# Kernel tuning notes

Measured on AMD Instinct MI355X. Metric: run time of the kernel, lower is better.

## Reference

```python
import jax, jax.numpy as jnp
import numpy as np
import math

H = 16        # num heads
D = 64        # head dim
HID = 1024    # hidden size
MULT = 2      # GIN MLP multiplier
FRAC = 0.1    # top_k fraction of available predecessors
THR = 0.2     # threshold value
BASE = 10000.0  # rope base
CHUNK = 32    # query-row chunk for max aggregator
NEG = -1e30


def _rope(x, pos):
    # x: (b, H, S, D); pos: (b, S) int
    d = x.shape[-1]
    inv = 1.0 / (BASE ** (jnp.arange(0, d, 2, dtype=jnp.float32) / d))
    ang = pos.astype(jnp.float32)[..., None] * inv            # (b, S, d//2)
    cos = jnp.concatenate([jnp.cos(ang)] * 2, -1)[:, None]    # (b, 1, S, d)
    sin = jnp.concatenate([jnp.sin(ang)] * 2, -1)[:, None]
    x1, x2 = jnp.split(x, 2, axis=-1)
    return x * cos + jnp.concatenate([-x2, x1], -1) * sin


def _scaled_topk_causal(adj):
    # faithful vectorization of scaled_topk_causal_4d: per query row i, keep
    # top max(1, ceil(FRAC*i)) of the (threshold-filtered) strict predecessors.
    S = adj.shape[-1]
    j = jnp.arange(S)
    strict = j[None, :] < j[:, None]                           # (S, S) j < i
    # torch: filtered = a[:, :i] * (a >= thr)  -> below-threshold become 0
    filtered = jnp.where(strict, jnp.where(adj >= THR, adj, 0.0), NEG)
    order = jnp.argsort(-filtered, axis=-1)                    # descending, stable
    rank = jnp.argsort(order, axis=-1)                         # inverse permutation
    k = jnp.maximum(1, jnp.ceil(FRAC * jnp.arange(S, dtype=jnp.float32))).astype(jnp.int32)
    k = k.at[0].set(0)                                         # row 0 has no predecessors
    return ((rank < k[None, None, :, None]) & strict).astype(adj.dtype)


def reference(hidden_states, Wq, Wk, Wv, Wo, W1, W2, eps, position_ids):
    b, S, _ = hidden_states.shape
    q = (hidden_states @ Wq).reshape(b, S, H, D).transpose(0, 2, 1, 3)
    kk = (hidden_states @ Wk).reshape(b, S, H, D).transpose(0, 2, 1, 3)
    v = (hidden_states @ Wv).reshape(b, S, H, D).transpose(0, 2, 1, 3)
    q = _rope(q, position_ids)
    kk = _rope(kk, position_ids)
    scores = jnp.einsum('bhid,bhjd->bhij', q, kk) / math.sqrt(D)
    adj = _scaled_topk_causal(scores)                          # binary (b,H,S,S)
    deg = adj.sum(-1)                                          # (b,H,S)
    denom = jnp.maximum(deg, 1.0)[..., None]
    s_agg = jnp.einsum('bhij,bhjd->bhid', adj, v)              # sum
    m_agg = s_agg / denom                                      # mean
    var = jnp.maximum(jnp.einsum('bhij,bhjd->bhid', adj, v * v) / denom - m_agg ** 2, 0.0)
    # max aggregator: masked max over selected predecessors, chunked over rows
    nc = S // CHUNK
    adj_c = jnp.moveaxis(adj.reshape(b, H, nc, CHUNK, S), 2, 0)  # (nc,b,H,C,S)
    mx = jax.lax.map(
        lambda ac: jnp.max(jnp.where(ac[..., None] > 0, v[:, :, None, :, :], NEG), axis=-2),
        adj_c)                                                 # (nc,b,H,C,D)
    mx = jnp.moveaxis(mx, 0, 2).reshape(b, H, S, D)
    mx = jnp.where(deg[..., None] > 0, mx, 0.0)
    comb = jnp.concatenate([s_agg, m_agg, mx, var], -1)        # (b,H,S,4D)
    h1 = jax.nn.silu(jnp.einsum('bhsf,hfm->bhsm', comb, W1))   # per-head GIN MLP
    head_out = jnp.einsum('bhsm,hmd->bhsd', h1, W2) + eps * v  # epsilon-scaled residual
    return head_out.transpose(0, 2, 1, 3).reshape(b, S, H * D) @ Wo


def setup_inputs() -> dict:
    key = jax.random.key(0)
    ks = jax.random.split(key, 8)
    b, S = 1, 1024
    sc = 0.02
    return {
        'hidden_states': jax.random.normal(ks[0], (b, S, HID), jnp.float32),
        'Wq': jax.random.normal(ks[1], (HID, H * D), jnp.float32) * sc,
        'Wk': jax.random.normal(ks[2], (HID, H * D), jnp.float32) * sc,
        'Wv': jax.random.normal(ks[3], (HID, H * D), jnp.float32) * sc,
        'Wo': jax.random.normal(ks[4], (H * D, HID), jnp.float32) * sc,
        'W1': jax.random.normal(ks[5], (H, 4 * D, MULT * D), jnp.float32) * sc,
        'W2': jax.random.normal(ks[6], (H, MULT * D, D), jnp.float32) * sc,
        'eps': jnp.asarray(0.1, jnp.float32),
        'position_ids': jnp.arange(S, dtype=jnp.int32)[None, :],
    }
```

## Files before the change

kernel.cpp:

```cpp
#include <hip/hip_runtime.h>
#include <math.h>

#define NEGF  -1e30f
#define TAU   1e-6f

static __device__ __forceinline__ int imin(int a, int b) { return a < b ? a : b; }

static __device__ __forceinline__ void fma44(float A[4][4], const float4 xa, const float4 yb) {
  A[0][0] += xa.x * yb.x; A[0][1] += xa.x * yb.y; A[0][2] += xa.x * yb.z; A[0][3] += xa.x * yb.w;
  A[1][0] += xa.y * yb.x; A[1][1] += xa.y * yb.y; A[1][2] += xa.y * yb.z; A[1][3] += xa.y * yb.w;
  A[2][0] += xa.z * yb.x; A[2][1] += xa.z * yb.y; A[2][2] += xa.z * yb.z; A[2][3] += xa.z * yb.w;
  A[3][0] += xa.w * yb.x; A[3][1] += xa.w * yb.y; A[3][2] += xa.w * yb.z; A[3][3] += xa.w * yb.w;
}

static __device__ __forceinline__ void fold44(float T[4][4], float A[4][4]) {
#pragma unroll
  for (int e = 0; e < 4; ++e)
#pragma unroll
    for (int f = 0; f < 4; ++f) { T[e][f] = __fadd_rn(T[e][f], A[e][f]); A[e][f] = 0.0f; }
}

template <int MODE>
__global__ __launch_bounds__(256) void gemm64(
    const float* __restrict__ A, const float* __restrict__ B, float* __restrict__ C,
    const float* __restrict__ R, const float* __restrict__ eps_p,
    int M, int N, int K, int lda, int ldb, int ldc,
    long sA, long sB, long sC)
{
  const int z = blockIdx.z;
  A += (long)z * sA;
  B += (long)z * sB;
  float* Cf = C + (long)z * sC;
  const float* Rz = (MODE == 2) ? (R + (long)z * sC) : nullptr;

  const int bm = blockIdx.x * 64;
  const int bn = blockIdx.y * 64;
  const int tid = threadIdx.x;
  const int r0 = (tid >> 4) * 4;
  const int c0 = (tid & 15) * 4;

  __shared__ float As[16][68];
  __shared__ float Bs[16][64];

  float acc[4][4] = {};

  const int ar = tid >> 2;
  const int ac = (tid & 3) * 4;
  const int br = tid >> 4;
  const int bc = (tid & 15) * 4;

  for (int kt = 0; kt < K; kt += 16) {
    float4 av = *(const float4*)(A + (long)(bm + ar) * lda + kt + ac);
    float4 bv = *(const float4*)(B + (long)(kt + br) * ldb + bn + bc);
    As[ac + 0][ar] = av.x;
    As[ac + 1][ar] = av.y;
    As[ac + 2][ar] = av.z;
    As[ac + 3][ar] = av.w;
    *(float4*)&Bs[br][bc] = bv;
    __syncthreads();
#pragma unroll
    for (int kk = 0; kk < 16; ++kk) {
      const float4 xa = *(const float4*)&As[kk][r0];
      const float4 yb = *(const float4*)&Bs[kk][c0];
      fma44(acc, xa, yb);
    }
    __syncthreads();
  }

  const float ev = (MODE == 2) ? eps_p[0] : 0.0f;
#pragma unroll
  for (int e = 0; e < 4; ++e)
#pragma unroll
    for (int f = 0; f < 4; ++f) {
      const int r = bm + r0 + e;
      const int c = bn + c0 + f;
      float x = acc[e][f];
      if (MODE == 1) x = x / (1.0f + expf(-x));
      if (MODE == 2) x += ev * Rz[(long)r * ldc + c];
      Cf[(long)r * ldc + c] = x;
    }
}

__global__ __launch_bounds__(256) void gemm_qkv_s48(
    const float* __restrict__ A,
    const float* __restrict__ Wq, const float* __restrict__ Wk, const float* __restrict__ Wv,
    float* __restrict__ part)
{
  const int z = blockIdx.z;
  const int mat = z % 3;
  const int panel = z / 3;
  const float* B = (mat == 0) ? Wq : (mat == 1) ? Wk : Wv;
  float* P = part + ((long)(mat * 3 + panel) << 20);

  const int k0 = panel * 384;
  const int k1 = (panel == 2) ? 1024 : (k0 + 384);

  const int bm = blockIdx.x * 64;
  const int bn = blockIdx.y * 128;
  const int tid = threadIdx.x;
  const int r0 = (tid >> 4) * 4;
  const int c0 = (tid & 15) * 4;

  __shared__ float As[2][16][68];
  __shared__ float Bs[2][16][132];

  float aL[4][4] = {}, aR[4][4] = {};

  const int ar = tid >> 2;
  const int ac = (tid & 3) * 4;
  const int br = tid >> 4;
  const int bc = (tid & 15) * 4;

  {
    float4 av = *(const float4*)(A + (long)(bm + ar) * 1024 + k0 + ac);
    float4 b0 = *(const float4*)(B + (long)(k0 + br) * 1024 + bn + bc);
    float4 b1 = *(const float4*)(B + (long)(k0 + br) * 1024 + bn + bc + 64);
    As[0][ac + 0][ar] = av.x; As[0][ac + 1][ar] = av.y;
    As[0][ac + 2][ar] = av.z; As[0][ac + 3][ar] = av.w;
    *(float4*)&Bs[0][br][bc] = b0;
    *(float4*)&Bs[0][br][bc + 64] = b1;
  }
  __syncthreads();

  int cur = 0;
  for (int kt = k0; kt < k1; kt += 16) {
    const bool more = (kt + 16 < k1);
    float4 avn, b0n, b1n;
    if (more) {
      avn = *(const float4*)(A + (long)(bm + ar) * 1024 + kt + 16 + ac);
      b0n = *(const float4*)(B + (long)(kt + 16 + br) * 1024 + bn + bc);
      b1n = *(const float4*)(B + (long)(kt + 16 + br) * 1024 + bn + bc + 64);
    }
#pragma unroll
    for (int kk = 0; kk < 16; ++kk) {
      const float4 xa = *(const float4*)&As[cur][kk][r0];
      const float4 y0 = *(const float4*)&Bs[cur][kk][c0];
      const float4 y1 = *(const float4*)&Bs[cur][kk][64 + c0];
      fma44(aL, xa, y0);
      fma44(aR, xa, y1);
    }
    if (more) {
      const int nxt = cur ^ 1;
      As[nxt][ac + 0][ar] = avn.x; As[nxt][ac + 1][ar] = avn.y;
      As[nxt][ac + 2][ar] = avn.z; As[nxt][ac + 3][ar] = avn.w;
      *(float4*)&Bs[nxt][br][bc] = b0n;
      *(float4*)&Bs[nxt][br][bc + 64] = b1n;
      __syncthreads();
      cur = nxt;
    }
  }

#pragma unroll
  for (int e = 0; e < 4; ++e) {
    float* prow = P + (long)(bm + r0 + e) * 1024 + bn;
#pragma unroll
    for (int f = 0; f < 4; ++f) {
      prow[c0 + f]      = aL[e][f];
      prow[64 + c0 + f] = aR[e][f];
    }
  }
}

__global__ __launch_bounds__(256) void combine_rope(
    const float4* __restrict__ part, const float2* __restrict__ tab,
    float4* __restrict__ q, float4* __restrict__ k, float4* __restrict__ v)
{
  const int g = blockIdx.x * 256 + threadIdx.x;
  if (g < 262144) {
    const int buf = g >> 17;
    const int rem = g & 131071;
    const int s   = rem >> 7;
    const int hx  = (rem >> 3) & 15;
    const int t4  = rem & 7;
    const int w   = s * 256 + hx * 16 + t4;
    const long b  = (long)(buf * 3) << 18;

    const float4 a0 = part[b + w];
    const float4 a1 = part[b + (1L << 18) + w];
    const float4 a2 = part[b + (2L << 18) + w];
    const float4 c0 = part[b + w + 8];
    const float4 c1 = part[b + (1L << 18) + w + 8];
    const float4 c2 = part[b + (2L << 18) + w + 8];

    float lo[4], hi[4];
    lo[0] = __fadd_rn(__fadd_rn(a0.x, a1.x), a2.x);
    lo[1] = __fadd_rn(__fadd_rn(a0.y, a1.y), a2.y);
    lo[2] = __fadd_rn(__fadd_rn(a0.z, a1.z), a2.z);
    lo[3] = __fadd_rn(__fadd_rn(a0.w, a1.w), a2.w);
    hi[0] = __fadd_rn(__fadd_rn(c0.x, c1.x), c2.x);
    hi[1] = __fadd_rn(__fadd_rn(c0.y, c1.y), c2.y);
    hi[2] = __fadd_rn(__fadd_rn(c0.z, c1.z), c2.z);
    hi[3] = __fadd_rn(__fadd_rn(c0.w, c1.w), c2.w);

    float ol[4], oh[4];
#pragma unroll
    for (int c = 0; c < 4; ++c) {
      const int t = t4 * 4 + c;
      const float2 cs = tab[s * 32 + t];
      const float x1 = lo[c];
      const float x2 = hi[c];
      ol[c] = __fadd_rn(__fmul_rn(x1, cs.x), __fmul_rn(-x2, cs.y));
      oh[c] = __fadd_rn(__fmul_rn(x2, cs.x), __fmul_rn(x1, cs.y));
    }
    float4* dst = buf ? k : q;
    dst[w]     = make_float4(ol[0], ol[1], ol[2], ol[3]);
    dst[w + 8] = make_float4(oh[0], oh[1], oh[2], oh[3]);
  } else {
    const int w = g - 262144;
    const long b = (long)6 << 18;
    const float4 s0 = part[b + w];
    const float4 s1 = part[b + (1L << 18) + w];
    const float4 s2 = part[b + (2L << 18) + w];
    float4 r;
    r.x = __fadd_rn(__fadd_rn(s0.x, s1.x), s2.x);
    r.y = __fadd_rn(__fadd_rn(s0.y, s1.y), s2.y);
    r.z = __fadd_rn(__fadd_rn(s0.z, s1.z), s2.z);
    r.w = __fadd_rn(__fadd_rn(s0.w, s1.w), s2.w);
    v[w] = r;
  }
}

__global__ __launch_bounds__(256) void combine_out(
    const float4* __restrict__ p, float4* __restrict__ dst)
{
  const int idx = blockIdx.x * 256 + threadIdx.x;
  const float4 a = p[idx];
  const float4 b = p[idx + (1 << 18)];
  float4 r;
  r.x = __fadd_rn(a.x, b.x);
  r.y = __fadd_rn(a.y, b.y);
  r.z = __fadd_rn(a.z, b.z);
  r.w = __fadd_rn(a.w, b.w);
  dst[idx] = r;
}

__global__ __launch_bounds__(256) void gemm_qkv64(
    const float* __restrict__ A,
    const float* __restrict__ Wq, const float* __restrict__ Wk, const float* __restrict__ Wv,
    float* __restrict__ qo, float* __restrict__ ko, float* __restrict__ vo)
{
  const int z = blockIdx.z;
  const float* B = (z == 0) ? Wq : (z == 1) ? Wk : Wv;
  float* C = (z == 0) ? qo : (z == 1) ? ko : vo;

  const int bm = blockIdx.x * 64;
  const int bn = blockIdx.y * 64;
  const int tid = threadIdx.x;
  const int r0 = (tid >> 4) * 4;
  const int c0 = (tid & 15) * 4;

  __shared__ float As[2][32][68];
  __shared__ float Bs[2][32][64];

  float acc[4][4] = {};
  float tot[4][4] = {};

  const int ar = tid >> 2;
  const int ac = (tid & 3) * 8;
  const int br = tid >> 3;
  const int bc = (tid & 7) * 8;

  {
    float4 a0 = *(const float4*)(A + (long)(bm + ar) * 1024 + ac);
    float4 a1 = *(const float4*)(A + (long)(bm + ar) * 1024 + ac + 4);
    float4 b0 = *(const float4*)(B + (long)br * 1024 + bn + bc);
    float4 b1 = *(const float4*)(B + (long)br * 1024 + bn + bc + 4);
    As[0][ac + 0][ar] = a0.x; As[0][ac + 1][ar] = a0.y;
    As[0][ac + 2][ar] = a0.z; As[0][ac + 3][ar] = a0.w;
    As[0][ac + 4][ar] = a1.x; As[0][ac + 5][ar] = a1.y;
    As[0][ac + 6][ar] = a1.z; As[0][ac + 7][ar] = a1.w;
    *(float4*)&Bs[0][br][bc] = b0;
    *(float4*)&Bs[0][br][bc + 4] = b1;
  }
  __syncthreads();

  int cur = 0;
  for (int kt = 0; kt < 1024; kt += 32) {
    const bool more = (kt + 32 < 1024);
    float4 a0n, a1n, b0n, b1n;
    if (more) {
      a0n = *(const float4*)(A + (long)(bm + ar) * 1024 + kt + 32 + ac);
      a1n = *(const float4*)(A + (long)(bm + ar) * 1024 + kt + 32 + ac + 4);
      b0n = *(const float4*)(B + (long)(kt + 32 + br) * 1024 + bn + bc);
      b1n = *(const float4*)(B + (long)(kt + 32 + br) * 1024 + bn + bc + 4);
    }
    if (kt == 384 || kt == 768) {
      fold44(tot, acc);
    }
#pragma unroll
    for (int kk = 0; kk < 32; ++kk) {
      const float4 xa = *(const float4*)&As[cur][kk][r0];
      const float4 yb = *(const float4*)&Bs[cur][kk][c0];
      fma44(acc, xa, yb);
    }
    if (more) {
      const int nxt = cur ^ 1;
      As[nxt][ac + 0][ar] = a0n.x; As[nxt][ac + 1][ar] = a0n.y;
      As[nxt][ac + 2][ar] = a0n.z; As[nxt][ac + 3][ar] = a0n.w;
      As[nxt][ac + 4][ar] = a1n.x; As[nxt][ac + 5][ar] = a1n.y;
      As[nxt][ac + 6][ar] = a1n.z; As[nxt][ac + 7][ar] = a1n.w;
      *(float4*)&Bs[nxt][br][bc] = b0n;
      *(float4*)&Bs[nxt][br][bc + 4] = b1n;
      __syncthreads();
      cur = nxt;
    }
  }

#pragma unroll
  for (int e = 0; e < 4; ++e)
#pragma unroll
    for (int f = 0; f < 4; ++f)
      C[(long)(bm + r0 + e) * 1024 + bn + c0 + f] = __fadd_rn(tot[e][f], acc[e][f]);
}

__global__ __launch_bounds__(256) void rope_table(
    const int* __restrict__ pos_ids, float2* __restrict__ tab)
{
  const int g = blockIdx.x * 256 + threadIdx.x;
  const int t = g & 31;
  const int s = g >> 5;

  const float e = (float)(2 * t) / 64.0f;
  const float p32 = (float)pow(10000.0, (double)e);
  const float inv = __fdiv_rn(1.0f, p32);
  const float posf = (float)pos_ids[s];
  const float ang = __fmul_rn(posf, inv);
  tab[g] = make_float2((float)cos((double)ang), (float)sin((double)ang));
}

__global__ __launch_bounds__(256) void rope_apply(float* __restrict__ q,
                                                  float* __restrict__ kb,
                                                  const float2* __restrict__ tab)
{
  const int g = blockIdx.x * blockDim.x + threadIdx.x;
  const int t = g & 31;
  const int h = (g >> 5) & 15;
  const int s = (g >> 9) & 1023;
  const int buf = g >> 19;
  float* p = buf ? kb : q;

  const float2 cs = tab[s * 32 + t];
  const float c  = cs.x;
  const float sn = cs.y;

  const int base = s * 1024 + h * 64;
  const float x1 = p[base + t];
  const float x2 = p[base + t + 32];
  p[base + t]      = __fadd_rn(__fmul_rn(x1, c), __fmul_rn(-x2, sn));
  p[base + t + 32] = __fadd_rn(__fmul_rn(x2, c), __fmul_rn(x1, sn));
}

__global__ __launch_bounds__(256) void gemm_score(
    const float* __restrict__ q, const float* __restrict__ kb,
    float* __restrict__ S, int headBase)
{
  const int x = blockIdx.x;
  int bmT = 0;
  while ((bmT + 1) * (bmT + 2) / 2 <= x) ++bmT;
  const int bnT = x - bmT * (bmT + 1) / 2;

  const int hl = blockIdx.y;
  const int off = (headBase + hl) * 64;
  const int bm = bmT * 64;
  const int bn = bnT * 64;
  const int tid = threadIdx.x;
  const int r0 = (tid >> 4) * 4;
  const int c0 = (tid & 15) * 4;

  __shared__ float As[16][68];
  __shared__ float Bs[16][68];

  float acc[4][4] = {};

  const int ar = tid >> 2;
  const int ac = (tid & 3) * 4;

  for (int kt = 0; kt < 64; kt += 16) {
    float4 av = *(const float4*)(q  + (long)(bm + ar) * 1024 + off + kt + ac);
    float4 bv = *(const float4*)(kb + (long)(bn + ar) * 1024 + off + kt + ac);
    As[ac + 0][ar] = av.x; As[ac + 1][ar] = av.y;
    As[ac + 2][ar] = av.z; As[ac + 3][ar] = av.w;
    Bs[ac + 0][ar] = bv.x; Bs[ac + 1][ar] = bv.y;
    Bs[ac + 2][ar] = bv.z; Bs[ac + 3][ar] = bv.w;
    __syncthreads();
#pragma unroll
    for (int kk = 0; kk < 16; ++kk) {
      const float4 xa = *(const float4*)&As[kk][r0];
      const float4 yb = *(const float4*)&Bs[kk][c0];
      fma44(acc, xa, yb);
    }
    __syncthreads();
  }

#pragma unroll
  for (int e = 0; e < 4; ++e)
#pragma unroll
    for (int f = 0; f < 4; ++f)
      S[((long)hl * 1024 + bm + r0 + e) * 1024 + bn + c0 + f] = acc[e][f] * 0.125f;
}

#define UFV(m) ((raw[m] >= 0.2f) ? __float_as_uint(raw[m]) : 0u)

__global__ __launch_bounds__(256) void select_agg6(
    const float* __restrict__ S, const float* __restrict__ v,
    float* __restrict__ comb, int headBase)
{
  const int tid = threadIdx.x;
  const int lane = tid & 63;
  const int wid = tid >> 6;
  const int i = blockIdx.x * 4 + wid;
  const int hl = blockIdx.y;
  const int h = headBase + hl;

  __shared__ int histS[4][256];
  __shared__ unsigned listS[4][128];
  int* hist = histS[wid];
  unsigned* list = listS[wid];

  const int nlayer = (i + 63) >> 6;
  const unsigned long long ltm = (1ull << lane) - 1ull;

  const float* row = S + ((long)hl * 1024 + i) * 1024;
  float raw[16];
#pragma unroll
  for (int m = 0; m < 16; ++m) raw[m] = 0.0f;
#pragma unroll
  for (int m = 0; m < 16; ++m) {
    if (m < nlayer) {
      const int j = m * 64 + lane;
      if (j < i) raw[m] = row[j];
    }
  }

  const int kk = (i > 0) ? (i + 9) / 10 : 0;
  unsigned V = 0u;
  int need_eq = 0;
  unsigned fmask = 0u;

  if (kk > 0) {
    int c3E = 0, c3F = 0, cHI = 0;
    bool anyBig = false;
#pragma unroll
    for (int m = 0; m < 16; ++m) {
      if (m < nlayer) {
        const unsigned u = UFV(m);
        if (u != 0u) {
          const unsigned tb = u >> 24;
          if (tb == 0x3Eu) ++c3E;
          else if (tb == 0x3Fu) ++c3F;
          else { ++cHI; if (tb > 0x40u) anyBig = true; }
        }
      }
    }
    const bool fastOK = (__ballot(anyBig) == 0ull);
    unsigned pk = (unsigned)c3E | ((unsigned)c3F << 10) | ((unsigned)cHI << 20);
#pragma unroll
    for (int off = 1; off < 64; off <<= 1)
      pk += (unsigned)__shfl_xor((int)pk, off, 64);
    const int t3E = (int)(pk & 1023u);
    const int t3F = (int)((pk >> 10) & 1023u);
    const int tHI = (int)((pk >> 20) & 1023u);
    const int totNZ = t3E + t3F + tHI;

    unsigned prefix = 0;
    int rk = kk;
    bool done = false;
    for (int pass = 0; pass < 4 && !done; ++pass) {
      const int shift = 24 - 8 * pass;
      if (pass == 0 && fastOK) {
        if (totNZ < rk) {
          V = 0u; need_eq = rk - totNZ; done = true;
        } else {
          int selBin, scnt;
          if (tHI >= rk)            { selBin = 0x40; scnt = tHI; }
          else if (tHI + t3F >= rk) { selBin = 0x3F; scnt = t3F; rk -= tHI; }
          else                      { selBin = 0x3E; scnt = t3E; rk -= tHI + t3F; }
          prefix = (unsigned)selBin;
          if (rk == scnt) {
            unsigned vm = 0xFFFFFFFFu;
#pragma unroll
            for (int m = 0; m < 16; ++m) {
              if (m < nlayer) {
                const unsigned u = UFV(m);
                if (u != 0u && (u >> shift) == prefix && u < vm) vm = u;
              }
            }
#pragma unroll
            for (int off = 1; off < 64; off <<= 1) {
              const unsigned o = (unsigned)__shfl_xor((int)vm, off, 64);
              if (o < vm) vm = o;
            }
            V = vm; need_eq = 0x3FFFFFFF; done = true;
          }
        }
        continue;
      }
      *(int4*)&hist[lane * 4] = make_int4(0, 0, 0, 0);
      asm volatile("s_waitcnt lgkmcnt(0)" ::: "memory");
      __builtin_amdgcn_sched_barrier(0);
#pragma unroll
      for (int m = 0; m < 16; ++m) {
        if (m < nlayer) {
          const unsigned u = UFV(m);
          if (u != 0u && (pass == 0 || (u >> (shift + 8)) == prefix))
            atomicAdd(&hist[(u >> shift) & 0xFF], 1);
        }
      }
      asm volatile("s_waitcnt lgkmcnt(0)" ::: "memory");
      __builtin_amdgcn_sched_barrier(0);
      const int4 hv = *(const int4*)&hist[lane * 4];
      const int s = hv.x + hv.y + hv.z + hv.w;
      int suf = s;
#pragma unroll
      for (int off = 1; off < 64; off <<= 1) {
        const int o = __shfl_down(suf, off, 64);
        if (lane + off < 64) suf += o;
      }
      const int tot = __shfl(suf, 0, 64);
      if (pass == 0 && tot < rk) {
        V = 0u; need_eq = rk - tot; done = true;
      } else {
        const int above = suf - s;
        const int sfx3 = above + hv.w;
        const int sfx2 = sfx3 + hv.z;
        const int sfx1 = sfx2 + hv.y;
        const int sfx0 = suf;
        int mbin = -1, mh = 0, msfx = 0;
        if (!(pass == 0 && lane == 0) && sfx0 >= rk && sfx0 - hv.x < rk) { mbin = lane * 4 + 0; mh = hv.x; msfx = sfx0; }
        if (sfx1 >= rk && sfx1 - hv.y < rk) { mbin = lane * 4 + 1; mh = hv.y; msfx = sfx1; }
        if (sfx2 >= rk && sfx2 - hv.z < rk) { mbin = lane * 4 + 2; mh = hv.z; msfx = sfx2; }
        if (sfx3 >= rk && sfx3 - hv.w < rk) { mbin = lane * 4 + 3; mh = hv.w; msfx = sfx3; }
        const unsigned long long bal = __ballot(mbin >= 0);
        const int src = (int)__ffsll((unsigned long long)bal) - 1;
        const int selBin = __shfl(mbin, src, 64) & 0xFF;
        const int scnt = __shfl(mh, src, 64);
        const int ssfx = __shfl(msfx, src, 64);
        prefix = (prefix << 8) | (unsigned)selBin;
        rk = rk - (ssfx - scnt);
        if (rk == scnt) {
          unsigned vm = 0xFFFFFFFFu;
#pragma unroll
          for (int m = 0; m < 16; ++m) {
            if (m < nlayer) {
              const unsigned u = UFV(m);
              if (u != 0u && (u >> shift) == prefix && u < vm) vm = u;
            }
          }
#pragma unroll
          for (int off = 1; off < 64; off <<= 1) {
            const unsigned o = (unsigned)__shfl_xor((int)vm, off, 64);
            if (o < vm) vm = o;
          }
          V = vm; need_eq = 0x3FFFFFFF; done = true;
        }
      }
    }
    if (!done) { V = prefix; need_eq = rk; }

    int prefEq = 0;
#pragma unroll
    for (int m = 0; m < 16; ++m) {
      if (m < nlayer) {
        const int j = m * 64 + lane;
        const bool validm = (j < i);
        const unsigned u = UFV(m);
        const bool eq = validm && (u == V);
        const unsigned long long bal = __ballot(eq);
        if (validm) {
          if (u > V) fmask |= (1u << m);
          else if (eq) {
            const int excl = prefEq + __popcll(bal & ltm);
            if (excl < need_eq) fmask |= (1u << m);
          }
        }
        prefEq += (int)__popcll(bal);
      }
    }
  }

  int hypOut = -1, hypIn = -1;
  if (kk > 0 && kk < i) {
    unsigned wmax = 0u;
    int mIn = -1;
    unsigned long long tbIn = ~0ull, tbOut = ~0ull;
#pragma unroll
    for (int m = 0; m < 16; ++m) {
      if (m < nlayer) {
        const int j = m * 64 + lane;
        if (j < i) {
          const unsigned u = UFV(m);
          if ((fmask >> m) & 1u) {
            if (u == V && j > mIn) mIn = j;
            const float fv = __uint_as_float(u);
            const float dd = fv - 0.2f;
            if (fv >= 0.2f && dd < TAU) {
              const unsigned long long p = (((unsigned long long)__float_as_uint(dd)) << 32) | (unsigned)j;
              if (p < tbIn) tbIn = p;
            }
          } else {
            if (u > wmax) wmax = u;
            if (raw[m] < 0.2f) {
              const float dd = 0.2f - raw[m];
              if (dd < TAU) {
                const unsigned long long p = (((unsigned long long)__float_as_uint(dd)) << 32) | (unsigned)j;
                if (p < tbOut) tbOut = p;
              }
            }
          }
        }
      }
    }
#pragma unroll
    for (int off = 1; off < 64; off <<= 1) {
      const unsigned ow = (unsigned)__shfl_xor((int)wmax, off, 64);
      if (ow > wmax) wmax = ow;
      const int om = __shfl_xor(mIn, off, 64);
      if (om > mIn) mIn = om;
      const unsigned long long oi = __shfl_xor(tbIn, off, 64);
      if (oi < tbIn) tbIn = oi;
      const unsigned long long oo = __shfl_xor(tbOut, off, 64);
      if (oo < tbOut) tbOut = oo;
    }
    int outMin = 0x7FFFFFFF;
#pragma unroll
    for (int m = 0; m < 16; ++m) {
      if (m < nlayer) {
        const int j = m * 64 + lane;
        if (j < i && !((fmask >> m) & 1u) && UFV(m) == wmax) {
          if (j < outMin) outMin = j;
        }
      }
    }
#pragma unroll
    for (int off = 1; off < 64; off <<= 1) {
      const int o = __shfl_xor(outMin, off, 64);
      if (o < outMin) outMin = o;
    }
    float bestD = TAU;
    int oI = -1, nI = -1;
    if (outMin != 0x7FFFFFFF && mIn >= 0) {
      const float Vf = __uint_as_float(V);
      const float Wf = __uint_as_float(wmax);
      if (!(wmax == V && V == 0u)) {
        const float gapA = Vf - Wf;
        if (gapA < bestD) { bestD = gapA; oI = mIn; nI = outMin; }
      }
      if (tbIn != ~0ull) {
        const float d = __uint_as_float((unsigned)(tbIn >> 32));
        const int jj = (int)(tbIn & 0xFFFFFFFFu);
        const bool noop = (wmax == 0u && jj < outMin);
        if (!noop && d < bestD) { bestD = d; oI = jj; nI = outMin; }
      }
      if (tbOut != ~0ull && Vf <= 0.2f) {
        const float d = __uint_as_float((unsigned)(tbOut >> 32));
        const int jj = (int)(tbOut & 0xFFFFFFFFu);
        if (d < bestD) { bestD = d; oI = mIn; nI = jj; }
      }
    }
    hypOut = oI; hypIn = nI;
  }

  const bool amb = (hypOut >= 0);
  int base = 0;
#pragma unroll
  for (int m = 0; m < 16; ++m) {
    if (m < nlayer) {
      const int j = m * 64 + lane;
      const bool validm = (j < i);
      const unsigned f0b = (fmask >> m) & 1u;
      int s1 = (int)f0b;
      if (amb) { if (j == hypOut) s1 = 0; if (j == hypIn) s1 = 1; }
      const bool sel = validm && ((f0b | (unsigned)s1) != 0u);
      const unsigned long long bal = __ballot(sel);
      if (sel) {
        const int pos = base + (int)__popcll(bal & ltm);
        list[pos] = (unsigned)j | (f0b << 10) | ((unsigned)s1 << 11);
      }
      base += (int)__popcll(bal);
    }
  }
  const int L = base;
  asm volatile("s_waitcnt lgkmcnt(0)" ::: "memory");
  __builtin_amdgcn_sched_barrier(0);

  const float denom = (float)(kk > 0 ? kk : 1);
  const float* vcol = v + h * 64 + lane;
  float* crow = comb + ((long)(h * 1024 + i)) * 256;

  if (!amb) {
    float sum0 = 0, sq0 = 0, mx0 = NEGF;
    for (int e2 = 0; e2 < L; e2 += 4) {
      const uint4 en4 = *(const uint4*)&list[e2];
      float v0 = 0, v1 = 0, v2 = 0, v3 = 0;
      const bool b0 = (e2 + 0 < L), b1 = (e2 + 1 < L), b2 = (e2 + 2 < L), b3 = (e2 + 3 < L);
      if (b0) v0 = vcol[(long)(en4.x & 1023) * 1024];
      if (b1) v1 = vcol[(long)(en4.y & 1023) * 1024];
      if (b2) v2 = vcol[(long)(en4.z & 1023) * 1024];
      if (b3) v3 = vcol[(long)(en4.w & 1023) * 1024];
      if (b0) { sum0 += v0; sq0 += v0 * v0; mx0 = fmaxf(mx0, v0); }
      if (b1) { sum0 += v1; sq0 += v1 * v1; mx0 = fmaxf(mx0, v1); }
      if (b2) { sum0 += v2; sq0 += v2 * v2; mx0 = fmaxf(mx0, v2); }
      if (b3) { sum0 += v3; sq0 += v3 * v3; mx0 = fmaxf(mx0, v3); }
    }
    const float mean0 = sum0 / denom;
    const float var0 = fmaxf(sq0 / denom - mean0 * mean0, 0.0f);
    const float mx0o = (kk > 0) ? mx0 : 0.0f;
    crow[lane]       = sum0;
    crow[64 + lane]  = mean0;
    crow[128 + lane] = mx0o;
    crow[192 + lane] = var0;
  } else {
    float sum0 = 0, sq0 = 0, mx0 = NEGF, sum1 = 0, sq1 = 0, mx1 = NEGF;
    for (int e2 = 0; e2 < L; e2 += 4) {
      const uint4 en4 = *(const uint4*)&list[e2];
      const unsigned w0 = (e2 + 0 < L) ? en4.x : 0u;
      const unsigned w1 = (e2 + 1 < L) ? en4.y : 0u;
      const unsigned w2 = (e2 + 2 < L) ? en4.z : 0u;
      const unsigned w3 = (e2 + 3 < L) ? en4.w : 0u;
      float v0 = 0, v1 = 0, v2 = 0, v3 = 0;
      if (w0) v0 = vcol[(long)(w0 & 1023) * 1024];
      if (w1) v1 = vcol[(long)(w1 & 1023) * 1024];
      if (w2) v2 = vcol[(long)(w2 & 1023) * 1024];
      if (w3) v3 = vcol[(long)(w3 & 1023) * 1024];
      if (w0 & (1u << 10)) { sum0 += v0; sq0 += v0 * v0; mx0 = fmaxf(mx0, v0); }
      if (w0 & (1u << 11)) { sum1 += v0; sq1 += v0 * v0; mx1 = fmaxf(mx1, v0); }
      if (w1 & (1u << 10)) { sum0 += v1; sq0 += v1 * v1; mx0 = fmaxf(mx0, v1); }
      if (w1 & (1u << 11)) { sum1 += v1; sq1 += v1 * v1; mx1 = fmaxf(mx1, v1); }
      if (w2 & (1u << 10)) { sum0 += v2; sq0 += v2 * v2; mx0 = fmaxf(mx0, v2); }
      if (w2 & (1u << 11)) { sum1 += v2; sq1 += v2 * v2; mx1 = fmaxf(mx1, v2); }
      if (w3 & (1u << 10)) { sum0 += v3; sq0 += v3 * v3; mx0 = fmaxf(mx0, v3); }
      if (w3 & (1u << 11)) { sum1 += v3; sq1 += v3 * v3; mx1 = fmaxf(mx1, v3); }
    }
    const float mean0 = sum0 / denom, mean1 = sum1 / denom;
    const float var0 = fmaxf(sq0 / denom - mean0 * mean0, 0.0f);
    const float var1 = fmaxf(sq1 / denom - mean1 * mean1, 0.0f);
    const float mx0o = (kk > 0) ? mx0 : 0.0f;
    const float mx1o = (kk > 0) ? mx1 : 0.0f;
    crow[lane]       = 0.5f * (sum0 + sum1);
    crow[64 + lane]  = 0.5f * (mean0 + mean1);
    crow[128 + lane] = 0.5f * (mx0o + mx1o);
    crow[192 + lane] = 0.5f * (var0 + var1);
  }
}

extern "C" void kernel_launch(void* const* d_in, const int* in_sizes, int n_in,
                              void* d_out, int out_size, void* d_ws, size_t ws_size,
                              hipStream_t stream)
{
  const float* hidden = (const float*)d_in[0];
  const float* Wq = (const float*)d_in[1];
  const float* Wk = (const float*)d_in[2];
  const float* Wv = (const float*)d_in[3];
  const float* Wo = (const float*)d_in[4];
  const float* W1 = (const float*)d_in[5];
  const float* W2 = (const float*)d_in[6];
  const float* eps = (const float*)d_in[7];
  const int* pos = (const int*)d_in[8];

  const size_t MB = 1024UL * 1024UL;
  int G = 4;
  if (ws_size >= 28 * MB + 64 * MB) G = 16;
  else if (ws_size >= 28 * MB + 32 * MB) G = 8;

  float* q      = (float*)d_ws;
  float* kbuf   = q + (1 << 20);
  float* v      = kbuf + (1 << 20);
  float* comb   = v + (1 << 20);
  float* scores = comb + (1 << 22);
  float* h1     = scores;
  float* ho     = scores + (1 << 21);
  float2* tab   = (float2*)comb;
  float* parts  = comb;

  const dim3 blk(256);

  rope_table<<<128, blk, 0, stream>>>(pos, tab);

  if (ws_size >= 64 * MB) {
    float* part = scores;
    gemm_qkv_s48<<<dim3(16, 8, 9), blk, 0, stream>>>(hidden, Wq, Wk, Wv, part);
    combine_rope<<<2048, blk, 0, stream>>>((const float4*)part, tab,
                                           (float4*)q, (float4*)kbuf, (float4*)v);
  } else {
    gemm_qkv64<<<dim3(16, 16, 3), blk, 0, stream>>>(hidden, Wq, Wk, Wv, q, kbuf, v);
    rope_apply<<<4096, blk, 0, stream>>>(q, kbuf, tab);
  }

  for (int g = 0; g < 16; g += G) {
    gemm_score<<<dim3(136, G), blk, 0, stream>>>(q, kbuf, scores, g);
    select_agg6<<<dim3(256, G), blk, 0, stream>>>(scores, v, comb, g);
  }

  gemm64<1><<<dim3(16, 2, 16), blk, 0, stream>>>(comb, W1, h1, nullptr, nullptr,
      1024, 128, 256, 256, 128, 128, (long)1024 * 256, (long)256 * 128, (long)1024 * 128);

  gemm64<2><<<dim3(16, 1, 16), blk, 0, stream>>>(h1, W2, ho, v, eps,
      1024, 64, 128, 128, 64, 1024, (long)1024 * 128, (long)128 * 64, 64);

  gemm64<0><<<dim3(16, 16, 2), blk, 0, stream>>>(ho, Wo, parts, nullptr, nullptr,
      1024, 1024, 512, 1024, 1024, 1024, 512, (long)512 * 1024, (long)1 << 20);
  combine_out<<<dim3(1024), blk, 0, stream>>>((const float4*)parts, (float4*)d_out);
}
```

Baseline: 333.2 us.

## Fuse per-head GIN MLP into one kernel and split Wo GEMM four ways

Replaces the two per-head GEMM launches (W1 with SiLU, then W2 with the eps residual) by one kernel. It keeps the SiLU hidden tile for 32 rows in shared memory and double-buffers the W1 operand loads, so the h1 intermediate never goes through global memory and one launch is dropped. The output projection now splits K into four parts instead of two, giving more blocks, and a four-way combine sums them. The trade-offs are more partial-sum traffic, a larger shared-memory footprint per block, and a different floating-point summation order.

```diff
diff --git a/kernel.cpp b/kernel.cpp
--- a/kernel.cpp
+++ b/kernel.cpp
@@ -11,6 +11,11 @@
   A[1][0] += xa.y * yb.x; A[1][1] += xa.y * yb.y; A[1][2] += xa.y * yb.z; A[1][3] += xa.y * yb.w;
   A[2][0] += xa.z * yb.x; A[2][1] += xa.z * yb.y; A[2][2] += xa.z * yb.z; A[2][3] += xa.z * yb.w;
   A[3][0] += xa.w * yb.x; A[3][1] += xa.w * yb.y; A[3][2] += xa.w * yb.z; A[3][3] += xa.w * yb.w;
+}
+
+static __device__ __forceinline__ void fma24(float A[2][4], const float2 xa, const float4 yb) {
+  A[0][0] += xa.x * yb.x; A[0][1] += xa.x * yb.y; A[0][2] += xa.x * yb.z; A[0][3] += xa.x * yb.w;
+  A[1][0] += xa.y * yb.x; A[1][1] += xa.y * yb.y; A[1][2] += xa.y * yb.z; A[1][3] += xa.y * yb.w;
 }
 
 static __device__ __forceinline__ void fold44(float T[4][4], float A[4][4]) {
@@ -78,6 +83,107 @@
       if (MODE == 1) x = x / (1.0f + expf(-x));
       if (MODE == 2) x += ev * Rz[(long)r * ldc + c];
       Cf[(long)r * ldc + c] = x;
+    }
+}
+
+__global__ __launch_bounds__(256) void gin_fused(
+    const float* __restrict__ comb, const float* __restrict__ W1,
+    const float* __restrict__ W2, const float* __restrict__ v,
+    const float* __restrict__ eps_p, float* __restrict__ ho)
+{
+  const int bm = blockIdx.x * 32;
+  const int h = blockIdx.y;
+  const float* A = comb + (long)h * 1024 * 256;
+  const float* B1 = W1 + (long)h * 256 * 128;
+  const float* B2 = W2 + (long)h * 128 * 64;
+
+  const int tid = threadIdx.x;
+  const int r0 = (tid >> 4) * 2;
+  const int c0 = (tid & 15) * 4;
+
+  __shared__ float As[2][16][36];
+  __shared__ float Bs[2][16][132];
+  __shared__ float H[128][36];
+  __shared__ float Bs2[16][68];
+
+  float aL[2][4] = {}, aR[2][4] = {};
+
+  const int ar = tid >> 3;
+  const int ac = (tid & 7) * 2;
+  const int br = tid >> 4;
+  const int bc = (tid & 15) * 4;
+
+  {
+    float2 av = *(const float2*)(A + (long)(bm + ar) * 256 + ac);
+    float4 b0 = *(const float4*)(B1 + (long)br * 128 + bc);
+    float4 b1 = *(const float4*)(B1 + (long)br * 128 + bc + 64);
+    As[0][ac + 0][ar] = av.x;
+    As[0][ac + 1][ar] = av.y;
+    *(float4*)&Bs[0][br][bc] = b0;
+    *(float4*)&Bs[0][br][bc + 64] = b1;
+  }
+  __syncthreads();
+
+  int cur = 0;
+  for (int kt = 0; kt < 256; kt += 16) {
+    const bool more = (kt + 16 < 256);
+    float2 avn;
+    float4 b0n, b1n;
+    if (more) {
+      avn = *(const float2*)(A + (long)(bm + ar) * 256 + kt + 16 + ac);
+      b0n = *(const float4*)(B1 + (long)(kt + 16 + br) * 128 + bc);
+      b1n = *(const float4*)(B1 + (long)(kt + 16 + br) * 128 + bc + 64);
+    }
+#pragma unroll
+    for (int kk = 0; kk < 16; ++kk) {
+      const float2 xa = *(const float2*)&As[cur][kk][r0];
+      const float4 y0 = *(const float4*)&Bs[cur][kk][c0];
+      const float4 y1 = *(const float4*)&Bs[cur][kk][64 + c0];
+      fma24(aL, xa, y0);
+      fma24(aR, xa, y1);
+    }
+    if (more) {
+      const int nxt = cur ^ 1;
+      As[nxt][ac + 0][ar] = avn.x;
+      As[nxt][ac + 1][ar] = avn.y;
+      *(float4*)&Bs[nxt][br][bc] = b0n;
+      *(float4*)&Bs[nxt][br][bc + 64] = b1n;
+      __syncthreads();
+      cur = nxt;
+    }
+  }
+
+#pragma unroll
+  for (int e = 0; e < 2; ++e)
+#pragma unroll
+    for (int f = 0; f < 4; ++f) {
+      const float xl = aL[e][f];
+      const float xr = aR[e][f];
+      H[c0 + f][r0 + e]      = xl / (1.0f + expf(-xl));
+      H[64 + c0 + f][r0 + e] = xr / (1.0f + expf(-xr));
+    }
+  __syncthreads();
+
+  float acc2[2][4] = {};
+  for (int kt = 0; kt < 128; kt += 16) {
+    *(float4*)&Bs2[br][bc] = *(const float4*)(B2 + (long)(kt + br) * 64 + bc);
+    __syncthreads();
+#pragma unroll
+    for (int kk = 0; kk < 16; ++kk) {
+      const float2 xa = *(const float2*)&H[kt + kk][r0];
+      const float4 yb = *(const float4*)&Bs2[kk][c0];
+      fma24(acc2, xa, yb);
+    }
+    __syncthreads();
+  }
+
+  const float ev = eps_p[0];
+#pragma unroll
+  for (int e = 0; e < 2; ++e)
+#pragma unroll
+    for (int f = 0; f < 4; ++f) {
+      const long idx = (long)(bm + r0 + e) * 1024 + h * 64 + c0 + f;
+      ho[idx] = acc2[e][f] + ev * v[idx];
     }
 }
 
@@ -220,17 +326,19 @@
   }
 }
 
-__global__ __launch_bounds__(256) void combine_out(
+__global__ __launch_bounds__(256) void combine_out4(
     const float4* __restrict__ p, float4* __restrict__ dst)
 {
   const int idx = blockIdx.x * 256 + threadIdx.x;
   const float4 a = p[idx];
   const float4 b = p[idx + (1 << 18)];
+  const float4 c = p[idx + (2 << 18)];
+  const float4 d = p[idx + (3 << 18)];
   float4 r;
-  r.x = __fadd_rn(a.x, b.x);
-  r.y = __fadd_rn(a.y, b.y);
-  r.z = __fadd_rn(a.z, b.z);
-  r.w = __fadd_rn(a.w, b.w);
+  r.x = __fadd_rn(__fadd_rn(__fadd_rn(a.x, b.x), c.x), d.x);
+  r.y = __fadd_rn(__fadd_rn(__fadd_rn(a.y, b.y), c.y), d.y);
+  r.z = __fadd_rn(__fadd_rn(__fadd_rn(a.z, b.z), c.z), d.z);
+  r.w = __fadd_rn(__fadd_rn(__fadd_rn(a.w, b.w), c.w), d.w);
   dst[idx] = r;
 }
 
@@ -767,7 +875,6 @@
   float* v      = kbuf + (1 << 20);
   float* comb   = v + (1 << 20);
   float* scores = comb + (1 << 22);
-  float* h1     = scores;
   float* ho     = scores + (1 << 21);
   float2* tab   = (float2*)comb;
   float* parts  = comb;
@@ -791,13 +898,9 @@
     select_agg6<<<dim3(256, G), blk, 0, stream>>>(scores, v, comb, g);
   }
 
-  gemm64<1><<<dim3(16, 2, 16), blk, 0, stream>>>(comb, W1, h1, nullptr, nullptr,
-      1024, 128, 256, 256, 128, 128, (long)1024 * 256, (long)256 * 128, (long)1024 * 128);
-
-  gemm64<2><<<dim3(16, 1, 16), blk, 0, stream>>>(h1, W2, ho, v, eps,
-      1024, 64, 128, 128, 64, 1024, (long)1024 * 128, (long)128 * 64, 64);
-
-  gemm64<0><<<dim3(16, 16, 2), blk, 0, stream>>>(ho, Wo, parts, nullptr, nullptr,
-      1024, 1024, 512, 1024, 1024, 1024, 512, (long)512 * 1024, (long)1 << 20);
-  combine_out<<<dim3(1024), blk, 0, stream>>>((const float4*)parts, (float4*)d_out);
-}
+  gin_fused<<<dim3(32, 16), blk, 0, stream>>>(comb, W1, W2, v, eps, ho);
+
+  gemm64<0><<<dim3(16, 16, 4), blk, 0, stream>>>(ho, Wo, parts, nullptr, nullptr,
+      1024, 1024, 256, 1024, 1024, 1024, 256, (long)256 * 1024, (long)1 << 20);
+  combine_out4<<<dim3(1024), blk, 0, stream>>>((const float4*)parts, (float4*)d_out);
+}
```

Measured after the change: 343.0 us. 1.03x slower.
